# Performance work log

Hardware: AMD Instinct MI355X
Metric: run time of the kernel (lower is better)

The kernel has to match this reference:

```python
import jax, jax.numpy as jnp
import numpy as np

D_MODEL = 2048
NHEADS = 16
NOPE = 128
ROPE = 64
VDIM = 128
QLORA = 1536
KVLORA = 512
QHD = NOPE + ROPE  # 192
B, T = 1, 4096


def rms_norm(x, w):
    # torch.nn.RMSNorm with eps=None uses finfo(dtype).eps
    eps = jnp.finfo(x.dtype).eps
    var = jnp.mean(x * x, axis=-1, keepdims=True)
    return x * jax.lax.rsqrt(var + eps) * w


def rope_cos_sin(T, dim):
    freqs = 1.0 / (10000.0 ** (jnp.arange(0, dim, 2, dtype=jnp.float32) / dim))
    ang = jnp.arange(T, dtype=jnp.float32)[:, None] * freqs[None, :]  # (T, dim/2)
    return jnp.cos(ang), jnp.sin(ang)


def apply_rope(x, cos, sin):
    # interleaved RoPE: even/odd channel pairs rotated
    xe = x[..., 0::2]
    xo = x[..., 1::2]
    re = xe * cos - xo * sin
    ro = xo * cos + xe * sin
    return jnp.stack([re, ro], axis=-1).reshape(x.shape)


def setup_inputs() -> dict:
    key = jax.random.key(0)
    ks = jax.random.split(key, 6)
    s = 0.02
    return {
        "x": jax.random.normal(ks[0], (B, T, D_MODEL), jnp.float32),
        "Wqa": jax.random.normal(ks[1], (D_MODEL, QLORA), jnp.float32) * s,
        "q_ln_w": jnp.ones((QLORA,), jnp.float32),
        "Wqb": jax.random.normal(ks[2], (QLORA, NHEADS * QHD), jnp.float32) * s,
        "Wkva": jax.random.normal(ks[3], (D_MODEL, KVLORA + ROPE), jnp.float32) * s,
        "kv_ln_w": jnp.ones((KVLORA,), jnp.float32),
        "Wkvb": jax.random.normal(ks[4], (KVLORA, NHEADS * (NOPE + VDIM)), jnp.float32) * s,
        "Wo": jax.random.normal(ks[5], (NHEADS * VDIM, D_MODEL), jnp.float32) * s,
    }


def reference(x, Wqa, q_ln_w, Wqb, Wkva, kv_ln_w, Wkvb, Wo):
    Bx, Tx, _ = x.shape
    cos, sin = rope_cos_sin(Tx, ROPE)  # (T, ROPE/2)

    # Low-rank Q path
    q = rms_norm(x @ Wqa, q_ln_w) @ Wqb
    q = q.reshape(Bx, Tx, NHEADS, QHD).transpose(0, 2, 1, 3)  # (B,H,T,QHD)
    q_nope = q[..., :NOPE]
    q_rope = apply_rope(q[..., NOPE:], cos, sin)  # (B,H,T,ROPE)

    # Compressed KV path + shared rope key
    kv = x @ Wkva
    kv_c = kv[..., :KVLORA]  # (B,T,KVLORA) latent cache
    k_rope = apply_rope(kv[..., KVLORA:], cos, sin)  # (B,T,ROPE), head-shared

    kvb = (rms_norm(kv_c, kv_ln_w) @ Wkvb).reshape(Bx, Tx, NHEADS, NOPE + VDIM)
    k_nope = kvb[..., :NOPE].transpose(0, 2, 1, 3)  # (B,H,T,NOPE)
    v = kvb[..., NOPE:].transpose(0, 2, 1, 3)       # (B,H,T,VDIM)

    # Scores split into nope part + head-shared rope part (avoids expanding k_rope to H heads)
    scale = 1.0 / jnp.sqrt(jnp.float32(QHD))
    s = jnp.einsum('bhqd,bhkd->bhqk', q_nope, k_nope)
    s = s + jnp.einsum('bhqd,bkd->bhqk', q_rope, k_rope)
    s = s * scale

    mask = jnp.tril(jnp.ones((Tx, Tx), dtype=bool))
    s = jnp.where(mask, s, -jnp.inf)
    a = jax.nn.softmax(s, axis=-1)

    o = jnp.einsum('bhqk,bhkd->bhqd', a, v)
    o = o.transpose(0, 2, 1, 3).reshape(Bx, Tx, NHEADS * VDIM)
    return o @ Wo
```

## Files before the change

### kernel.cpp

```cpp
#include <hip/hip_runtime.h>
#include <hip/hip_bf16.h>

typedef __attribute__((ext_vector_type(8))) short short8;
typedef __attribute__((ext_vector_type(4))) float f32x4;

#define GLDS16(gp, lp)                                                         \
  __builtin_amdgcn_global_load_lds(                                            \
      (const __attribute__((address_space(1))) void*)(gp),                     \
      (__attribute__((address_space(3))) void*)(lp), 16, 0, 0)

static __device__ __forceinline__ unsigned int pack_bf16(float a, float b) {
  __hip_bfloat16 ba = __float2bfloat16(a), bb = __float2bfloat16(b);
  unsigned short ua = *reinterpret_cast<unsigned short*>(&ba);
  unsigned short ub = *reinterpret_cast<unsigned short*>(&bb);
  return (unsigned int)ua | ((unsigned int)ub << 16);
}

static __device__ __forceinline__ int xcd_swz(int linear, int nwg) {
  return (linear & 7) * (nwg >> 3) + (linear >> 3);
}

__global__ __launch_bounds__(256) void cast_rope_kernel(
    const float* __restrict__ in, __hip_bfloat16* __restrict__ out, int n4,
    float* __restrict__ cs, float* __restrict__ sn)
{
  int i = blockIdx.x * 256 + threadIdx.x;
  if (i < n4) {
    float4 v = ((const float4*)in)[i];
    out[(size_t)i * 4 + 0] = __float2bfloat16(v.x);
    out[(size_t)i * 4 + 1] = __float2bfloat16(v.y);
    out[(size_t)i * 4 + 2] = __float2bfloat16(v.z);
    out[(size_t)i * 4 + 3] = __float2bfloat16(v.w);
  }
  if (blockIdx.x < 4096 && threadIdx.x < 32) {
    int t = blockIdx.x, j = threadIdx.x;
    float freq = powf(10000.f, -2.f * (float)j / 64.f);
    float ang = (float)t * freq;
    cs[t * 32 + j] = cosf(ang);
    sn[t * 32 + j] = sinf(ang);
  }
}

__global__ void transpose_all_kernel(
    const float* __restrict__ Wqa, const float* __restrict__ Wkva,
    const float* __restrict__ Wqb, const float* __restrict__ Wkvb,
    const float* __restrict__ Wo,
    __hip_bfloat16* __restrict__ WdownT, __hip_bfloat16* __restrict__ WqbT,
    __hip_bfloat16* __restrict__ WkvbT, __hip_bfloat16* __restrict__ WoT)
{
  __shared__ float tile[32][33];
  int b = blockIdx.x;
  const float* in;
  __hip_bfloat16* outp;
  int K, N, Npad, gx;
  if (b < 3072)        { in = Wqa;  outp = WdownT;                        K = 2048; N = 1536; Npad = 1536; gx = 48; }
  else if (b < 4352)   { b -= 3072; in = Wkva; outp = WdownT + (size_t)1536 * 2048; K = 2048; N = 576;  Npad = 640;  gx = 20; }
  else if (b < 8960)   { b -= 4352; in = Wqb;  outp = WqbT;               K = 1536; N = 3072; Npad = 3072; gx = 96; }
  else if (b < 11008)  { b -= 8960; in = Wkvb; outp = WkvbT;              K = 512;  N = 4096; Npad = 4096; gx = 128; }
  else                 { b -= 11008; in = Wo;  outp = WoT;                K = 2048; N = 2048; Npad = 2048; gx = 64; }
  int n0 = (b % gx) * 32, k0 = (b / gx) * 32;
  int tx = threadIdx.x, ty = threadIdx.y;
  #pragma unroll
  for (int i = ty; i < 32; i += 8) {
    int k = k0 + i, n = n0 + tx;
    tile[i][tx] = (n < N) ? in[(size_t)k * N + n] : 0.f;
  }
  __syncthreads();
  #pragma unroll
  for (int i = ty; i < 32; i += 8) {
    int n = n0 + i, k = k0 + tx;
    if (n < Npad) outp[(size_t)n * K + k] = __float2bfloat16(tile[tx][i]);
  }
}

#define GEMM_MAIN(A, BT, Kdim)                                                 \
  __shared__ __hip_bfloat16 As[128 * 32];                                      \
  __shared__ __hip_bfloat16 Bs[128 * 32];                                      \
  const int tid = threadIdx.x;                                                 \
  const int wave = tid >> 6, lane = tid & 63;                                  \
  const int wr = wave >> 1, wc = wave & 1;                                     \
  const int lq = lane & 15, grp = lane >> 4;                                   \
  const int nwg = gridDim.x * gridDim.y;                                       \
  const int orig = xcd_swz(blockIdx.y * gridDim.x + blockIdx.x, nwg);          \
  const int row0 = (orig / gridDim.x) * 128;                                   \
  const int col0 = (orig % gridDim.x) * 128;                                   \
  const f32x4 z4 = {0.f, 0.f, 0.f, 0.f};                                       \
  f32x4 acc[4][4];                                                             \
  _Pragma("unroll") for (int i = 0; i < 4; i++)                                \
      _Pragma("unroll") for (int j = 0; j < 4; j++) acc[i][j] = z4;            \
  for (int k0 = 0; k0 < (Kdim); k0 += 32) {                                    \
    _Pragma("unroll") for (int i = 0; i < 2; i++) {                            \
      const int t = wave + 4 * i;                                              \
      const int c = t * 64 + lane;                                             \
      const int cr = c >> 2;                                                   \
      const int ko = (c & 3) << 3;                                             \
      GLDS16((A) + (size_t)(row0 + cr) * (Kdim) + (k0 + ko), (char*)As + t * 1024); \
      GLDS16((BT) + (size_t)(col0 + cr) * (Kdim) + (k0 + ko), (char*)Bs + t * 1024);\
    }                                                                          \
    __syncthreads();                                                           \
    short8 af[4], bfr[4];                                                      \
    _Pragma("unroll") for (int mm = 0; mm < 4; mm++)                           \
      af[mm] = *(const short8*)((const short*)As + ((wr * 64 + mm * 16 + lq) * 32 + grp * 8)); \
    _Pragma("unroll") for (int nn = 0; nn < 4; nn++)                           \
      bfr[nn] = *(const short8*)((const short*)Bs + ((wc * 64 + nn * 16 + lq) * 32 + grp * 8));\
    _Pragma("unroll") for (int mm = 0; mm < 4; mm++)                           \
      _Pragma("unroll") for (int nn = 0; nn < 4; nn++)                         \
        acc[mm][nn] = __builtin_amdgcn_mfma_f32_16x16x32_bf16(af[mm], bfr[nn], acc[mm][nn], 0, 0, 0); \
    __syncthreads();                                                           \
  }

__global__ __launch_bounds__(256) void gemm_down_kernel(
    const __hip_bfloat16* __restrict__ A,
    const __hip_bfloat16* __restrict__ BT,
    float* __restrict__ q_lat, float* __restrict__ kvout)
{
  GEMM_MAIN(A, BT, 2048)
  #pragma unroll
  for (int mm = 0; mm < 4; mm++)
    #pragma unroll
    for (int nn = 0; nn < 4; nn++) {
      const int row = row0 + wr * 64 + mm * 16 + grp * 4;
      const int col = col0 + wc * 64 + nn * 16 + lq;
      float* Cp = (col < 1536) ? (q_lat + (size_t)row * 1536 + col)
                               : (kvout + (size_t)row * 640 + (col - 1536));
      const size_t ld = (col < 1536) ? 1536 : 640;
      #pragma unroll
      for (int rr = 0; rr < 4; rr++) Cp[(size_t)rr * ld] = acc[mm][nn][rr];
    }
}

#define GEMM256_MAIN(Aptr, BTptr, Kdim)                                        \
  __shared__ __align__(16) char Ab[2][32768];                                  \
  __shared__ __align__(16) char Bb[2][32768];                                  \
  const int tid = threadIdx.x;                                                 \
  const int wid = tid >> 6, lane = tid & 63;                                   \
  const int wm = wid >> 2, wn = wid & 3;                                       \
  const int lq = lane & 15, grp = lane >> 4;                                   \
  const int nwg = gridDim.x * gridDim.y;                                       \
  const int orig = xcd_swz(blockIdx.y * gridDim.x + blockIdx.x, nwg);          \
  const int row0 = (orig / gridDim.x) * 256;                                   \
  const int col0 = (orig % gridDim.x) * 256;                                   \
  const size_t K2 = (size_t)(Kdim) * 2;                                        \
  const char* pa[4]; const char* pb[4]; int ldst[4];                           \
  _Pragma("unroll") for (int i = 0; i < 4; i++) {                              \
    int L = i * 8192 + tid * 16;                                               \
    int r = L >> 7;                                                            \
    int csw = (L & 127) ^ ((r & 7) << 4);                                      \
    ldst[i] = L;                                                               \
    pa[i] = (const char*)(Aptr) + (size_t)(row0 + r) * K2 + csw;               \
    pb[i] = (const char*)(BTptr) + (size_t)(col0 + r) * K2 + csw;              \
  }                                                                            \
  const int xm = (lq & 7) << 4;                                                \
  const f32x4 z4 = {0.f, 0.f, 0.f, 0.f};                                       \
  f32x4 acc[8][4];                                                             \
  _Pragma("unroll") for (int i = 0; i < 8; i++)                                \
    _Pragma("unroll") for (int j = 0; j < 4; j++) acc[i][j] = z4;              \
  const int nt = (Kdim) >> 6;                                                  \
  _Pragma("unroll") for (int i = 0; i < 4; i++) {                              \
    GLDS16(pa[i], &Ab[0][0] + ldst[i]);                                        \
    GLDS16(pb[i], &Bb[0][0] + ldst[i]);                                        \
  }                                                                            \
  for (int t = 0; t < nt; ++t) {                                               \
    const int b = t & 1;                                                       \
    if (t + 1 < nt) {                                                          \
      const size_t koff = (size_t)(t + 1) * 128;                               \
      _Pragma("unroll") for (int i = 0; i < 4; i++) {                          \
        GLDS16(pa[i] + koff, &Ab[b ^ 1][0] + ldst[i]);                         \
        GLDS16(pb[i] + koff, &Bb[b ^ 1][0] + ldst[i]);                         \
      }                                                                        \
      asm volatile("s_waitcnt vmcnt(8)" ::: "memory");                         \
    } else {                                                                   \
      asm volatile("s_waitcnt vmcnt(0)" ::: "memory");                         \
    }                                                                          \
    __builtin_amdgcn_sched_barrier(0);                                         \
    __builtin_amdgcn_s_barrier();                                              \
    __builtin_amdgcn_sched_barrier(0);                                         \
    const char* Ar = &Ab[b][0];                                                \
    const char* Br = &Bb[b][0];                                                \
    short8 bfr[4][2];                                                          \
    _Pragma("unroll") for (int n = 0; n < 4; n++)                              \
      _Pragma("unroll") for (int ks = 0; ks < 2; ks++)                         \
        bfr[n][ks] = *(const short8*)(Br + (wn * 64 + n * 16 + lq) * 128 +     \
                                      ((ks * 64 + grp * 16) ^ xm));            \
    _Pragma("unroll") for (int mh = 0; mh < 4; mh++) {                         \
      short8 af[2][2];                                                         \
      _Pragma("unroll") for (int mi = 0; mi < 2; mi++)                         \
        _Pragma("unroll") for (int ks = 0; ks < 2; ks++)                       \
          af[mi][ks] = *(const short8*)(Ar + (wm * 128 + (mh * 2 + mi) * 16 + lq) * 128 + \
                                        ((ks * 64 + grp * 16) ^ xm));          \
      __builtin_amdgcn_s_setprio(1);                                           \
      _Pragma("unroll") for (int mi = 0; mi < 2; mi++)                         \
        _Pragma("unroll") for (int n = 0; n < 4; n++)                          \
          _Pragma("unroll") for (int ks = 0; ks < 2; ks++)                     \
            acc[mh * 2 + mi][n] = __builtin_amdgcn_mfma_f32_16x16x32_bf16(     \
                af[mi][ks], bfr[n][ks], acc[mh * 2 + mi][n], 0, 0, 0);         \
      __builtin_amdgcn_s_setprio(0);                                           \
    }                                                                          \
    __builtin_amdgcn_sched_barrier(0);                                         \
    __builtin_amdgcn_s_barrier();                                              \
    __builtin_amdgcn_sched_barrier(0);                                         \
  }

__global__ __launch_bounds__(512, 2) void gemm256_bt_kernel(
    const __hip_bfloat16* __restrict__ A,
    const __hip_bfloat16* __restrict__ BT,
    float* __restrict__ C, int N, int K)
{
  GEMM256_MAIN(A, BT, K)
  #pragma unroll
  for (int m = 0; m < 8; m++)
    #pragma unroll
    for (int n = 0; n < 4; n++) {
      const int row = row0 + wm * 128 + m * 16 + grp * 4;
      const int col = col0 + wn * 64 + n * 16 + lq;
      float* Cp = C + (size_t)row * N + col;
      #pragma unroll
      for (int rr = 0; rr < 4; rr++) Cp[(size_t)rr * N] = acc[m][n][rr];
    }
}

__global__ __launch_bounds__(512, 2) void gemm256_qup_kernel(
    const __hip_bfloat16* __restrict__ A,
    const __hip_bfloat16* __restrict__ BT,
    __hip_bfloat16* __restrict__ Qh,
    const float* __restrict__ cs_tab, const float* __restrict__ sn_tab, int K)
{
  GEMM256_MAIN(A, BT, K)
  const float scale = 0.10411654209f;
  #pragma unroll
  for (int m = 0; m < 8; m++)
    #pragma unroll
    for (int n = 0; n < 4; n++) {
      const int col = col0 + wn * 64 + n * 16 + lq;
      const int h = col / 192;
      const int d = col - h * 192;
      const bool is_rope = (d >= 128);
      const int i = (d - 128) >> 1;
      const float sgn = (d & 1) ? 1.f : -1.f;
      #pragma unroll
      for (int rr = 0; rr < 4; rr++) {
        const int t = row0 + wm * 128 + m * 16 + grp * 4 + rr;
        float val = acc[m][n][rr];
        float partner = __shfl_xor(val, 1);
        float outv = val;
        if (is_rope) {
          float c = cs_tab[t * 32 + i];
          float s = sn_tab[t * 32 + i];
          outv = val * c + sgn * partner * s;
        }
        Qh[((size_t)h * 4096 + t) * 192 + d] = __float2bfloat16(outv * scale);
      }
    }
}

__global__ __launch_bounds__(512, 2) void gemm256_kvup_kernel(
    const __hip_bfloat16* __restrict__ A,
    const __hip_bfloat16* __restrict__ BT,
    __hip_bfloat16* __restrict__ Kh,
    __hip_bfloat16* __restrict__ Vt, int K)
{
  GEMM256_MAIN(A, BT, K)
  #pragma unroll
  for (int m = 0; m < 8; m++)
    #pragma unroll
    for (int n = 0; n < 4; n++) {
      const int col = col0 + wn * 64 + n * 16 + lq;
      const int h = col >> 8;
      const int j = col & 255;
      const int t0 = row0 + wm * 128 + m * 16 + grp * 4;
      if (j < 128) {
        #pragma unroll
        for (int rr = 0; rr < 4; rr++)
          Kh[((size_t)h * 4096 + t0 + rr) * 192 + j] = __float2bfloat16(acc[m][n][rr]);
      } else {
        const int vd = j - 128;
        uint2 w;
        w.x = pack_bf16(acc[m][n][0], acc[m][n][1]);
        w.y = pack_bf16(acc[m][n][2], acc[m][n][3]);
        *(uint2*)(Vt + ((size_t)h * 128 + vd) * 4096 + t0) = w;
      }
    }
}

__global__ __launch_bounds__(256) void rmsnorm2_kernel(
    const float* __restrict__ q_lat, const float* __restrict__ kv,
    const float* __restrict__ qw, const float* __restrict__ kvw,
    __hip_bfloat16* __restrict__ q_ln, __hip_bfloat16* __restrict__ kv_ln,
    const float* __restrict__ cs_tab, const float* __restrict__ sn_tab,
    __hip_bfloat16* __restrict__ Kh)
{
  const int b = blockIdx.x;
  const bool isq = (b < 4096);
  const int row = isq ? b : b - 4096;
  const int ld = isq ? 1536 : 640;
  const int W = isq ? 1536 : 512;
  const float* x = (isq ? q_lat : kv) + (size_t)row * ld;
  const float* w = isq ? qw : kvw;
  __hip_bfloat16* out = (isq ? q_ln : kv_ln) + (size_t)row * W;
  const int tid = threadIdx.x;
  const int wave = tid >> 6, lane = tid & 63;
  float ss = 0.f;
  for (int i = tid; i < W; i += 256) { float v = x[i]; ss += v * v; }
  #pragma unroll
  for (int o = 32; o; o >>= 1) ss += __shfl_xor(ss, o);
  __shared__ float red[4];
  __shared__ float stot;
  if (lane == 0) red[wave] = ss;
  __syncthreads();
  if (tid == 0) stot = red[0] + red[1] + red[2] + red[3];
  __syncthreads();
  const float rstd = rsqrtf(stot / (float)W + 1.1920929e-7f);
  for (int i = tid; i < W; i += 256)
    out[i] = __float2bfloat16(x[i] * rstd * w[i]);
  if (!isq) {
    const int t = row;
    for (int e = tid; e < 512; e += 256) {
      int h = e >> 5, i = e & 31;
      float c = cs_tab[t * 32 + i], s = sn_tab[t * 32 + i];
      float xe = x[512 + 2 * i];
      float xo = x[512 + 2 * i + 1];
      size_t base = ((size_t)h * 4096 + t) * 192 + 128 + 2 * i;
      Kh[base]     = __float2bfloat16(xe * c - xo * s);
      Kh[base + 1] = __float2bfloat16(xo * c + xe * s);
    }
  }
}

__global__ __launch_bounds__(256, 2) void flash_attn_kernel(
    const __hip_bfloat16* __restrict__ Qh,
    const __hip_bfloat16* __restrict__ Kh,
    const __hip_bfloat16* __restrict__ Vt,
    __hip_bfloat16* __restrict__ Obf)
{
  __shared__ __align__(16) char Klds[2][24576];
  __shared__ __align__(16) char Vlds[2][16384];

  const int hw = blockIdx.x;
  const int rest = hw >> 3;
  const int h = (hw & 7) + 8 * (rest & 1);
  const int p = rest >> 1;

  const int wave = threadIdx.x >> 6;
  const int lane = threadIdx.x & 63;
  const int lq = lane & 15;
  const int grp = lane >> 4;
  const int qb_[2] = {(63 - p) * 64 + wave * 16,
                      p * 64 + wave * 16};
  const int kendA = qb_[0] + 16;
  const int kendB = qb_[1] + 16;
  const int nt = 64 - p;

  const char* Kh_ = (const char*)(Kh + (size_t)h * 4096 * 192);
  const char* Vh_ = (const char*)(Vt + (size_t)h * 128 * 4096);
  const short* Qh_ = (const short*)Qh + (size_t)h * 4096 * 192;

  int kbase[6], vbase[4];
  #pragma unroll
  for (int i = 0; i < 6; i++) {
    int L = (wave * 6 + i) * 1024 + lane * 16;
    int r = L / 384, c = L - r * 384;
    int swb = (r & 3) | (((r >> 3) & 1) << 2);
    kbase[i] = r * 384 + (c ^ (swb << 4));
  }
  #pragma unroll
  for (int i = 0; i < 4; i++) {
    int L = (wave * 4 + i) * 1024 + lane * 16;
    int r = L >> 7, c = L & 127;
    vbase[i] = r * 8192 + (c ^ ((r & 7) << 4));
  }

  short8 qf[2][6];
  #pragma unroll
  for (int f = 0; f < 2; f++)
    #pragma unroll
    for (int d = 0; d < 6; d++)
      qf[f][d] = *(const short8*)(Qh_ + (size_t)(qb_[f] + lq) * 192 + d * 32 + grp * 8);

  const f32x4 z4 = {0.f, 0.f, 0.f, 0.f};
  f32x4 o_acc[2][8];
  #pragma unroll
  for (int f = 0; f < 2; f++)
    #pragma unroll
    for (int v = 0; v < 8; v++) o_acc[f][v] = z4;
  float m[2] = {-1e30f, -1e30f};
  float lsum[2] = {0.f, 0.f};

  const int krow_l = ((lq >> 2) << 3) + (lq & 3);
  const int kxm = ((lq & 3) | (((lq >> 2) & 1) << 2)) << 4;
  const int vxm = (lq & 7) << 4;

  {
    #pragma unroll
    for (int i = 0; i < 6; i++) GLDS16(Kh_ + kbase[i], Klds[0] + (wave * 6 + i) * 1024);
    #pragma unroll
    for (int i = 0; i < 4; i++) GLDS16(Vh_ + vbase[i], Vlds[0] + (wave * 4 + i) * 1024);
  }

  for (int t = 0; t < nt; t++) {
    __syncthreads();
    if (t + 1 < nt) {
      const char* Kp = Kh_ + (size_t)(t + 1) * 64 * 384;
      const char* Vp = Vh_ + (size_t)(t + 1) * 128;
      char* Kd = Klds[(t + 1) & 1];
      char* Vd = Vlds[(t + 1) & 1];
      #pragma unroll
      for (int i = 0; i < 6; i++) GLDS16(Kp + kbase[i], Kd + (wave * 6 + i) * 1024);
      #pragma unroll
      for (int i = 0; i < 4; i++) GLDS16(Vp + vbase[i], Vd + (wave * 4 + i) * 1024);
    }
    const char* Kb = Klds[t & 1];
    const char* Vb = Vlds[t & 1];
    const int ks = t * 64;

    #pragma unroll
    for (int h2 = 0; h2 < 2; h2++) {
      const int ks32 = ks + h2 * 32;
      if (ks32 >= kendA) continue;
      const bool act1 = (ks32 < kendB);

      f32x4 st[2][2];
      #pragma unroll
      for (int kt = 0; kt < 2; kt++) {
        const int row = h2 * 32 + krow_l + kt * 4;
        short8 kf[6];
        #pragma unroll
        for (int d = 0; d < 6; d++)
          kf[d] = *(const short8*)(Kb + row * 384 + ((d * 64 + grp * 16) ^ kxm));
        __builtin_amdgcn_s_setprio(1);
        #pragma unroll
        for (int f = 0; f < 2; f++) {
          if (f == 1 && !act1) continue;
          f32x4 acc = z4;
          #pragma unroll
          for (int d = 0; d < 6; d++)
            acc = __builtin_amdgcn_mfma_f32_16x16x32_bf16(kf[d], qf[f][d], acc, 0, 0, 0);
          st[f][kt] = acc;
        }
        __builtin_amdgcn_s_setprio(0);
      }

      short8 vf[8];
      #pragma unroll
      for (int v = 0; v < 8; v++)
        vf[v] = *(const short8*)(Vb + (v * 16 + lq) * 128 + ((h2 * 64 + grp * 16) ^ vxm));

      #pragma unroll
      for (int f = 0; f < 2; f++) {
        if (f == 1 && !act1) continue;
        const int qg = qb_[f] + lq;
        const bool need_mask = (ks32 + 31 > qb_[f]);
        if (need_mask) {
          #pragma unroll
          for (int kt = 0; kt < 2; kt++)
            #pragma unroll
            for (int r = 0; r < 4; r++) {
              int key = ks32 + grp * 8 + kt * 4 + r;
              if (key > qg) st[f][kt][r] = -1e30f;
            }
        }
        float tmax = fmaxf(fmaxf(fmaxf(st[f][0][0], st[f][0][1]), fmaxf(st[f][0][2], st[f][0][3])),
                           fmaxf(fmaxf(st[f][1][0], st[f][1][1]), fmaxf(st[f][1][2], st[f][1][3])));
        tmax = fmaxf(tmax, __shfl_xor(tmax, 16));
        tmax = fmaxf(tmax, __shfl_xor(tmax, 32));
        if (!__all(tmax <= m[f] + 11.5416f)) {
          float mnew = fmaxf(m[f], tmax);
          float alpha = exp2f(m[f] - mnew);
          m[f] = mnew;
          lsum[f] *= alpha;
          float a0 = __shfl(alpha, grp * 4 + 0);
          float a1 = __shfl(alpha, grp * 4 + 1);
          float a2 = __shfl(alpha, grp * 4 + 2);
          float a3 = __shfl(alpha, grp * 4 + 3);
          #pragma unroll
          for (int v = 0; v < 8; v++) {
            o_acc[f][v][0] *= a0; o_acc[f][v][1] *= a1;
            o_acc[f][v][2] *= a2; o_acc[f][v][3] *= a3;
          }
        }
        float p00 = exp2f(st[f][0][0] - m[f]), p01 = exp2f(st[f][0][1] - m[f]);
        float p02 = exp2f(st[f][0][2] - m[f]), p03 = exp2f(st[f][0][3] - m[f]);
        float p10 = exp2f(st[f][1][0] - m[f]), p11 = exp2f(st[f][1][1] - m[f]);
        float p12 = exp2f(st[f][1][2] - m[f]), p13 = exp2f(st[f][1][3] - m[f]);
        lsum[f] += ((p00 + p01) + (p02 + p03)) + ((p10 + p11) + (p12 + p13));
        union { unsigned int u[4]; short8 s8; } pu;
        pu.u[0] = pack_bf16(p00, p01);
        pu.u[1] = pack_bf16(p02, p03);
        pu.u[2] = pack_bf16(p10, p11);
        pu.u[3] = pack_bf16(p12, p13);
        short8 pa = pu.s8;
        __builtin_amdgcn_s_setprio(1);
        #pragma unroll
        for (int v = 0; v < 8; v++)
          o_acc[f][v] = __builtin_amdgcn_mfma_f32_16x16x32_bf16(pa, vf[v], o_acc[f][v], 0, 0, 0);
        __builtin_amdgcn_s_setprio(0);
      }
    }
  }

  #pragma unroll
  for (int f = 0; f < 2; f++) {
    float ls = lsum[f];
    ls += __shfl_xor(ls, 16);
    ls += __shfl_xor(ls, 32);
    float linv = 1.f / ls;
    float l0 = __shfl(linv, grp * 4 + 0);
    float l1 = __shfl(linv, grp * 4 + 1);
    float l2 = __shfl(linv, grp * 4 + 2);
    float l3 = __shfl(linv, grp * 4 + 3);
    const int qb = qb_[f];
    #pragma unroll
    for (int v = 0; v < 8; v++) {
      int col = h * 128 + v * 16 + lq;
      Obf[(size_t)(qb + grp * 4 + 0) * 2048 + col] = __float2bfloat16(o_acc[f][v][0] * l0);
      Obf[(size_t)(qb + grp * 4 + 1) * 2048 + col] = __float2bfloat16(o_acc[f][v][1] * l1);
      Obf[(size_t)(qb + grp * 4 + 2) * 2048 + col] = __float2bfloat16(o_acc[f][v][2] * l2);
      Obf[(size_t)(qb + grp * 4 + 3) * 2048 + col] = __float2bfloat16(o_acc[f][v][3] * l3);
    }
  }
}

extern "C" void kernel_launch(void* const* d_in, const int* in_sizes, int n_in,
                              void* d_out, int out_size, void* d_ws, size_t ws_size,
                              hipStream_t stream)
{
  (void)in_sizes; (void)n_in; (void)out_size; (void)ws_size;
  const float* x     = (const float*)d_in[0];
  const float* Wqa   = (const float*)d_in[1];
  const float* qlnw  = (const float*)d_in[2];
  const float* Wqb   = (const float*)d_in[3];
  const float* Wkva  = (const float*)d_in[4];
  const float* kvlnw = (const float*)d_in[5];
  const float* Wkvb  = (const float*)d_in[6];
  const float* Wo    = (const float*)d_in[7];
  float* out = (float*)d_out;
  char* ws = (char*)d_ws;

  size_t off = 0;
  auto take = [&](size_t bytes) {
    char* p = ws + off;
    off += (bytes + 255) & ~(size_t)255;
    return p;
  };

  __hip_bfloat16* x_bf   = (__hip_bfloat16*)take((size_t)4096 * 2048 * 2);
  __hip_bfloat16* WdownT = (__hip_bfloat16*)take((size_t)2176 * 2048 * 2);
  __hip_bfloat16* WqbT   = (__hip_bfloat16*)take((size_t)3072 * 1536 * 2);
  __hip_bfloat16* WkvbT  = (__hip_bfloat16*)take((size_t)4096 * 512 * 2);
  __hip_bfloat16* WoT    = (__hip_bfloat16*)take((size_t)2048 * 2048 * 2);
  char* regA             = take((size_t)4096 * 1536 * 4);
  float* kv              = (float*)take((size_t)4096 * 640 * 4);
  __hip_bfloat16* q_ln   = (__hip_bfloat16*)take((size_t)4096 * 1536 * 2);
  __hip_bfloat16* kv_ln  = (__hip_bfloat16*)take((size_t)4096 * 512 * 2);
  float* cs_tab          = (float*)take((size_t)4096 * 32 * 4);
  float* sn_tab          = (float*)take((size_t)4096 * 32 * 4);
  __hip_bfloat16* Khp    = (__hip_bfloat16*)take((size_t)16 * 4096 * 192 * 2);
  __hip_bfloat16* Vtp    = (__hip_bfloat16*)take((size_t)16 * 128 * 4096 * 2);
  __hip_bfloat16* o_bf   = (__hip_bfloat16*)take((size_t)4096 * 2048 * 2);

  float* q_lat = (float*)regA;
  __hip_bfloat16* Qh = (__hip_bfloat16*)regA;

  cast_rope_kernel<<<dim3(8192), 256, 0, stream>>>(x, x_bf, 2097152, cs_tab, sn_tab);
  transpose_all_kernel<<<dim3(15104), dim3(32, 8), 0, stream>>>(
      Wqa, Wkva, Wqb, Wkvb, Wo, WdownT, WqbT, WkvbT, WoT);

  gemm_down_kernel<<<dim3(17, 32), 256, 0, stream>>>(x_bf, WdownT, q_lat, kv);

  rmsnorm2_kernel<<<dim3(8192), 256, 0, stream>>>(q_lat, kv, qlnw, kvlnw, q_ln, kv_ln,
                                                  cs_tab, sn_tab, Khp);

  gemm256_qup_kernel<<<dim3(12, 16), 512, 0, stream>>>(q_ln, WqbT, Qh, cs_tab, sn_tab, 1536);
  gemm256_kvup_kernel<<<dim3(16, 16), 512, 0, stream>>>(kv_ln, WkvbT, Khp, Vtp, 512);

  flash_attn_kernel<<<dim3(512), 256, 0, stream>>>(Qh, Khp, Vtp, o_bf);

  gemm256_bt_kernel<<<dim3(8, 16), 512, 0, stream>>>(o_bf, WoT, out, 2048, 2048);
}
```

Before: 446.4 us.

## Fuse x cast with down-weight transpose and overlap up-weight transposes with down GEMM

The x cast/rope-table kernel is merged with the transpose of only the down-projection weights (Wqa, Wkva). The remaining weight transposes (Wqb, Wkvb, Wo) move into the down-projection GEMM launch as extra blocks, so they run alongside the GEMM tiles instead of as a separate serial pass. The output projection switches from the 256-tile pipelined GEMM to a simpler 128-tile GEMM with more blocks. This removes one launch and some serialization, but the final GEMM may be slower per FLOP, and the mixed launch pairs GEMM blocks with small transpose blocks.

```diff
diff --git a/kernel.cpp b/kernel.cpp
--- a/kernel.cpp
+++ b/kernel.cpp
@@ -20,46 +20,38 @@
   return (linear & 7) * (nwg >> 3) + (linear >> 3);
 }
 
-__global__ __launch_bounds__(256) void cast_rope_kernel(
-    const float* __restrict__ in, __hip_bfloat16* __restrict__ out, int n4,
+__global__ __launch_bounds__(256) void cast_tr_kernel(
+    const float* __restrict__ x, __hip_bfloat16* __restrict__ x_bf,
+    const float* __restrict__ Wqa, const float* __restrict__ Wkva,
+    __hip_bfloat16* __restrict__ WdownT,
     float* __restrict__ cs, float* __restrict__ sn)
-{
-  int i = blockIdx.x * 256 + threadIdx.x;
-  if (i < n4) {
-    float4 v = ((const float4*)in)[i];
-    out[(size_t)i * 4 + 0] = __float2bfloat16(v.x);
-    out[(size_t)i * 4 + 1] = __float2bfloat16(v.y);
-    out[(size_t)i * 4 + 2] = __float2bfloat16(v.z);
-    out[(size_t)i * 4 + 3] = __float2bfloat16(v.w);
-  }
-  if (blockIdx.x < 4096 && threadIdx.x < 32) {
-    int t = blockIdx.x, j = threadIdx.x;
-    float freq = powf(10000.f, -2.f * (float)j / 64.f);
-    float ang = (float)t * freq;
-    cs[t * 32 + j] = cosf(ang);
-    sn[t * 32 + j] = sinf(ang);
-  }
-}
-
-__global__ void transpose_all_kernel(
-    const float* __restrict__ Wqa, const float* __restrict__ Wkva,
-    const float* __restrict__ Wqb, const float* __restrict__ Wkvb,
-    const float* __restrict__ Wo,
-    __hip_bfloat16* __restrict__ WdownT, __hip_bfloat16* __restrict__ WqbT,
-    __hip_bfloat16* __restrict__ WkvbT, __hip_bfloat16* __restrict__ WoT)
 {
   __shared__ float tile[32][33];
   int b = blockIdx.x;
+  const int tid = threadIdx.x;
+  if (b < 8192) {
+    int i = b * 256 + tid;
+    float4 v = ((const float4*)x)[i];
+    x_bf[(size_t)i * 4 + 0] = __float2bfloat16(v.x);
+    x_bf[(size_t)i * 4 + 1] = __float2bfloat16(v.y);
+    x_bf[(size_t)i * 4 + 2] = __float2bfloat16(v.z);
+    x_bf[(size_t)i * 4 + 3] = __float2bfloat16(v.w);
+    if (b < 4096 && tid < 32) {
+      float freq = powf(10000.f, -2.f * (float)tid / 64.f);
+      float ang = (float)b * freq;
+      cs[b * 32 + tid] = cosf(ang);
+      sn[b * 32 + tid] = sinf(ang);
+    }
+    return;
+  }
+  b -= 8192;
   const float* in;
   __hip_bfloat16* outp;
   int K, N, Npad, gx;
-  if (b < 3072)        { in = Wqa;  outp = WdownT;                        K = 2048; N = 1536; Npad = 1536; gx = 48; }
-  else if (b < 4352)   { b -= 3072; in = Wkva; outp = WdownT + (size_t)1536 * 2048; K = 2048; N = 576;  Npad = 640;  gx = 20; }
-  else if (b < 8960)   { b -= 4352; in = Wqb;  outp = WqbT;               K = 1536; N = 3072; Npad = 3072; gx = 96; }
-  else if (b < 11008)  { b -= 8960; in = Wkvb; outp = WkvbT;              K = 512;  N = 4096; Npad = 4096; gx = 128; }
-  else                 { b -= 11008; in = Wo;  outp = WoT;                K = 2048; N = 2048; Npad = 2048; gx = 64; }
+  if (b < 3072) { in = Wqa;  outp = WdownT;                        K = 2048; N = 1536; Npad = 1536; gx = 48; }
+  else { b -= 3072; in = Wkva; outp = WdownT + (size_t)1536 * 2048; K = 2048; N = 576;  Npad = 640;  gx = 20; }
   int n0 = (b % gx) * 32, k0 = (b / gx) * 32;
-  int tx = threadIdx.x, ty = threadIdx.y;
+  int tx = tid & 31, ty = tid >> 5;
   #pragma unroll
   for (int i = ty; i < 32; i += 8) {
     int k = k0 + i, n = n0 + tx;
@@ -73,17 +65,10 @@
   }
 }
 
-#define GEMM_MAIN(A, BT, Kdim)                                                 \
-  __shared__ __hip_bfloat16 As[128 * 32];                                      \
-  __shared__ __hip_bfloat16 Bs[128 * 32];                                      \
-  const int tid = threadIdx.x;                                                 \
+#define GEMM128_CORE(A, BT, Kdim)                                              \
   const int wave = tid >> 6, lane = tid & 63;                                  \
   const int wr = wave >> 1, wc = wave & 1;                                     \
   const int lq = lane & 15, grp = lane >> 4;                                   \
-  const int nwg = gridDim.x * gridDim.y;                                       \
-  const int orig = xcd_swz(blockIdx.y * gridDim.x + blockIdx.x, nwg);          \
-  const int row0 = (orig / gridDim.x) * 128;                                   \
-  const int col0 = (orig % gridDim.x) * 128;                                   \
   const f32x4 z4 = {0.f, 0.f, 0.f, 0.f};                                       \
   f32x4 acc[4][4];                                                             \
   _Pragma("unroll") for (int i = 0; i < 4; i++)                                \
@@ -109,24 +94,86 @@
     __syncthreads();                                                           \
   }
 
-__global__ __launch_bounds__(256) void gemm_down_kernel(
+__global__ __launch_bounds__(256) void gemm_bt_kernel(
     const __hip_bfloat16* __restrict__ A,
     const __hip_bfloat16* __restrict__ BT,
-    float* __restrict__ q_lat, float* __restrict__ kvout)
-{
-  GEMM_MAIN(A, BT, 2048)
+    float* __restrict__ C, int M, int N, int K)
+{
+  __shared__ __hip_bfloat16 As[128 * 32];
+  __shared__ __hip_bfloat16 Bs[128 * 32];
+  const int tid = threadIdx.x;
+  const int nwg = gridDim.x * gridDim.y;
+  const int orig = xcd_swz(blockIdx.y * gridDim.x + blockIdx.x, nwg);
+  const int row0 = (orig / gridDim.x) * 128;
+  const int col0 = (orig % gridDim.x) * 128;
+  GEMM128_CORE(A, BT, K)
+  (void)M;
   #pragma unroll
   for (int mm = 0; mm < 4; mm++)
     #pragma unroll
     for (int nn = 0; nn < 4; nn++) {
       const int row = row0 + wr * 64 + mm * 16 + grp * 4;
       const int col = col0 + wc * 64 + nn * 16 + lq;
-      float* Cp = (col < 1536) ? (q_lat + (size_t)row * 1536 + col)
-                               : (kvout + (size_t)row * 640 + (col - 1536));
-      const size_t ld = (col < 1536) ? 1536 : 640;
-      #pragma unroll
-      for (int rr = 0; rr < 4; rr++) Cp[(size_t)rr * ld] = acc[mm][nn][rr];
-    }
+      float* Cp = C + (size_t)row * N + col;
+      #pragma unroll
+      for (int rr = 0; rr < 4; rr++) Cp[(size_t)rr * N] = acc[mm][nn][rr];
+    }
+}
+
+__global__ __launch_bounds__(256) void gemm_down_tr_kernel(
+    const __hip_bfloat16* __restrict__ A,
+    const __hip_bfloat16* __restrict__ BT,
+    float* __restrict__ q_lat, float* __restrict__ kvout,
+    const float* __restrict__ Wqb, const float* __restrict__ Wkvb,
+    const float* __restrict__ Wo,
+    __hip_bfloat16* __restrict__ WqbT, __hip_bfloat16* __restrict__ WkvbT,
+    __hip_bfloat16* __restrict__ WoT)
+{
+  __shared__ __align__(16) char smem[16512];
+  const int tid = threadIdx.x;
+  int b = blockIdx.x;
+  if (b < 544) {
+    __hip_bfloat16* As = (__hip_bfloat16*)smem;
+    __hip_bfloat16* Bs = (__hip_bfloat16*)(smem + 8192);
+    const int orig = xcd_swz(b, 544);
+    const int row0 = (orig / 17) * 128;
+    const int col0 = (orig % 17) * 128;
+    GEMM128_CORE(A, BT, 2048)
+    #pragma unroll
+    for (int mm = 0; mm < 4; mm++)
+      #pragma unroll
+      for (int nn = 0; nn < 4; nn++) {
+        const int row = row0 + wr * 64 + mm * 16 + grp * 4;
+        const int col = col0 + wc * 64 + nn * 16 + lq;
+        float* Cp = (col < 1536) ? (q_lat + (size_t)row * 1536 + col)
+                                 : (kvout + (size_t)row * 640 + (col - 1536));
+        const size_t ld = (col < 1536) ? 1536 : 640;
+        #pragma unroll
+        for (int rr = 0; rr < 4; rr++) Cp[(size_t)rr * ld] = acc[mm][nn][rr];
+      }
+    return;
+  }
+  b -= 544;
+  float (*tile)[33] = (float(*)[33])smem;
+  const float* in;
+  __hip_bfloat16* outp;
+  int K, N, Npad, gx;
+  if (b < 4608)      { in = Wqb;  outp = WqbT;  K = 1536; N = 3072; Npad = 3072; gx = 96; }
+  else if (b < 6656) { b -= 4608; in = Wkvb; outp = WkvbT; K = 512;  N = 4096; Npad = 4096; gx = 128; }
+  else               { b -= 6656; in = Wo;   outp = WoT;   K = 2048; N = 2048; Npad = 2048; gx = 64; }
+  int n0 = (b % gx) * 32, k0 = (b / gx) * 32;
+  int tx = tid & 31, ty = tid >> 5;
+  #pragma unroll
+  for (int i = ty; i < 32; i += 8) {
+    int k = k0 + i, n = n0 + tx;
+    tile[i][tx] = (n < N) ? in[(size_t)k * N + n] : 0.f;
+  }
+  __syncthreads();
+  #pragma unroll
+  for (int i = ty; i < 32; i += 8) {
+    int n = n0 + i, k = k0 + tx;
+    if (n < Npad) outp[(size_t)n * K + k] = __float2bfloat16(tile[tx][i]);
+  }
 }
 
 #define GEMM256_MAIN(Aptr, BTptr, Kdim)                                        \
@@ -201,24 +248,6 @@
     __builtin_amdgcn_sched_barrier(0);                                         \
   }
 
-__global__ __launch_bounds__(512, 2) void gemm256_bt_kernel(
-    const __hip_bfloat16* __restrict__ A,
-    const __hip_bfloat16* __restrict__ BT,
-    float* __restrict__ C, int N, int K)
-{
-  GEMM256_MAIN(A, BT, K)
-  #pragma unroll
-  for (int m = 0; m < 8; m++)
-    #pragma unroll
-    for (int n = 0; n < 4; n++) {
-      const int row = row0 + wm * 128 + m * 16 + grp * 4;
-      const int col = col0 + wn * 64 + n * 16 + lq;
-      float* Cp = C + (size_t)row * N + col;
-      #pragma unroll
-      for (int rr = 0; rr < 4; rr++) Cp[(size_t)rr * N] = acc[m][n][rr];
-    }
-}
-
 __global__ __launch_bounds__(512, 2) void gemm256_qup_kernel(
     const __hip_bfloat16* __restrict__ A,
     const __hip_bfloat16* __restrict__ BT,
@@ -560,11 +589,11 @@
   float* q_lat = (float*)regA;
   __hip_bfloat16* Qh = (__hip_bfloat16*)regA;
 
-  cast_rope_kernel<<<dim3(8192), 256, 0, stream>>>(x, x_bf, 2097152, cs_tab, sn_tab);
-  transpose_all_kernel<<<dim3(15104), dim3(32, 8), 0, stream>>>(
-      Wqa, Wkva, Wqb, Wkvb, Wo, WdownT, WqbT, WkvbT, WoT);
-
-  gemm_down_kernel<<<dim3(17, 32), 256, 0, stream>>>(x_bf, WdownT, q_lat, kv);
+  cast_tr_kernel<<<dim3(12544), 256, 0, stream>>>(x, x_bf, Wqa, Wkva, WdownT,
+                                                  cs_tab, sn_tab);
+
+  gemm_down_tr_kernel<<<dim3(11296), 256, 0, stream>>>(
+      x_bf, WdownT, q_lat, kv, Wqb, Wkvb, Wo, WqbT, WkvbT, WoT);
 
   rmsnorm2_kernel<<<dim3(8192), 256, 0, stream>>>(q_lat, kv, qlnw, kvlnw, q_ln, kv_ln,
                                                   cs_tab, sn_tab, Khp);
@@ -574,5 +603,5 @@
 
   flash_attn_kernel<<<dim3(512), 256, 0, stream>>>(Qh, Khp, Vtp, o_bf);
 
-  gemm256_bt_kernel<<<dim3(8, 16), 512, 0, stream>>>(o_bf, WoT, out, 2048, 2048);
-}
+  gemm_bt_kernel<<<dim3(16, 32), 256, 0, stream>>>(o_bf, WoT, out, 4096, 2048, 2048);
+}
```

Result: faster. 433.9 us (-2.8%).
